# Kernel tuning notes

Measured on AMD Instinct MI355X. Metric: run time of the kernel, lower is better.

The kernel has to match this reference:

```python
import jax, jax.numpy as jnp
import numpy as np

B, NCOL, NCOND = 1024, 64, 64
NRODT, D, NEST, NFOREST, NHID, NCLASS = 1024, 4, 128, 100, 128, 10
EPS = 1e-5


def setup_inputs() -> dict:
    key = jax.random.key(0)
    ks = jax.random.split(key, 16)
    rng = np.random.default_rng(0)
    s = 0.1
    inp = {
        'x': jax.random.normal(ks[0], (B, NCOL), jnp.float32),
        # phi_1 numerical grouped conv: groups=NCOL, in_per_g=1, out_per_g=NCOND
        'w1': jax.random.normal(ks[1], (NCOL, 1, NCOND), jnp.float32) * s,
        'b1': jax.random.normal(ks[2], (NCOL * NCOND,), jnp.float32) * s,
        # rODTConstruction fixed permutation of the 4096 conditions
        'perm': jnp.asarray(rng.permutation(NCOND * NCOL), jnp.int32),
        'gn1_g': jnp.ones((NCOND * NCOL,), jnp.float32),
        'gn1_b': jnp.zeros((NCOND * NCOL,), jnp.float32),
        # phi_2 grouped convs: groups=NRODT, block D->D then D->1
        'w2a': jax.random.normal(ks[3], (NRODT, D, D), jnp.float32) * s,
        'b2a': jax.random.normal(ks[4], (NRODT * D,), jnp.float32) * s,
        'gn2_g': jnp.ones((NCOND * NCOL,), jnp.float32),
        'gn2_b': jnp.zeros((NCOND * NCOL,), jnp.float32),
        'w2b': jax.random.normal(ks[5], (NRODT, D, 1), jnp.float32) * s,
        'b2b': jax.random.normal(ks[6], (NRODT,), jnp.float32) * s,
        'E': jax.random.normal(ks[7], (NRODT, NHID), jnp.float32) * s,
        # eval-mode sample_without_replacement buffer: per-forest subset of rODTs
        'swr': jnp.asarray(np.argsort(rng.random((NFOREST, NRODT)), axis=-1)[:, :NEST], jnp.int32),
        'ln1_g': jnp.ones((NHID,), jnp.float32),
        'ln1_b': jnp.zeros((NHID,), jnp.float32),
        'lin1_w': jax.random.normal(ks[8], (NHID, NHID), jnp.float32) * s,
        'lin1_b': jax.random.normal(ks[9], (NHID,), jnp.float32) * s,
        'ln2_g': jnp.ones((NHID,), jnp.float32),
        'ln2_b': jnp.zeros((NHID,), jnp.float32),
        'lin2_w': jax.random.normal(ks[10], (NHID, NCLASS), jnp.float32) * s,
        'lin2_b': jax.random.normal(ks[11], (NCLASS,), jnp.float32) * s,
    }
    return inp


def _group_norm(v, g, gamma, beta):
    # v: (B, C), normalize within each of g channel groups (L=1 in the torch module)
    b, c = v.shape
    vg = v.reshape(b, g, c // g)
    mu = vg.mean(-1, keepdims=True)
    var = vg.var(-1, keepdims=True)
    vn = ((vg - mu) / jnp.sqrt(var + EPS)).reshape(b, c)
    return vn * gamma + beta


def _layer_norm(v, gamma, beta):
    mu = v.mean(-1, keepdims=True)
    var = v.var(-1, keepdims=True)
    return (v - mu) / jnp.sqrt(var + EPS) * gamma + beta


def reference(x, w1, b1, perm, gn1_g, gn1_b, w2a, b2a, gn2_g, gn2_b, w2b, b2b,
              E, swr, ln1_g, ln1_b, lin1_w, lin1_b, ln2_g, ln2_b, lin2_w, lin2_b):
    b = x.shape[0]
    # ConditionGeneration (numerical only): block-diag GEMV with in_per_group=1
    M = jax.nn.sigmoid(x[:, :, None] * w1[None, :, 0, :] + b1.reshape(NCOL, NCOND))  # (B, NCOL, NCOND)
    M = M.transpose(0, 2, 1)  # (B, NCOND, NCOL)
    # rODTConstruction: flatten + fixed permutation
    O = M.reshape(b, NCOND * NCOL)[:, perm]  # (B, 4096)
    # phi_2: GroupNorm -> grouped conv (D->D) -> ReLU -> GroupNorm -> grouped conv (D->1)
    h = _group_norm(O, NRODT, gn1_g, gn1_b).reshape(b, NRODT, D)
    h = jnp.einsum('bgi,gio->bgo', h, w2a) + b2a.reshape(NRODT, D)
    h = jax.nn.relu(h).reshape(b, NRODT * D)
    h = _group_norm(h, NRODT, gn2_g, gn2_b).reshape(b, NRODT, D)
    w = jnp.einsum('bgi,gio->bgo', h, w2b)[..., 0] + b2b  # (B, NRODT), n_head=1
    # forest construction: gather rODT subsets, softmax over estimators, weighted embed sum
    ws = jax.nn.softmax(w[:, swr], axis=-1)  # (B, NFOREST, NEST)
    Es = E[swr]  # (NFOREST, NEST, NHID)
    F = jnp.einsum('bfe,feh->bfh', ws, Es)  # (B, NFOREST, NHID)
    # phi_3 bagging MLP (eval mode: dropout = identity)
    z = _layer_norm(F, ln1_g, ln1_b)
    z = jax.nn.relu(z @ lin1_w + lin1_b)
    z = _layer_norm(z, ln2_g, ln2_b)
    y_hats = z @ lin2_w + lin2_b  # (B, NFOREST, NCLASS)
    return y_hats.mean(1)  # (B, NCLASS)
```

## Files before the change

### kernel.cpp

```cpp
#include <hip/hip_runtime.h>


#define B_      1024
#define NCOL_   64
#define NCOND_  64
#define NRODT_  1024
#define NEST_   128
#define NFOREST_ 100
#define NHID_   128
#define NCLASS_ 10
#define EPS_    1e-5f

typedef __bf16 bf16_t;
typedef bf16_t bf16x8 __attribute__((ext_vector_type(8)));
typedef float  f32x4  __attribute__((ext_vector_type(4)));

#define MFMA16(a,b,c) __builtin_amdgcn_mfma_f32_16x16x32_bf16(a,b,c,0,0,0)

#define EG_FRAGS   (NFOREST_*4*8*64)
#define W1_FRAGS   (4*8*64)
#define L2_FRAGS   (4*64)

#define ZLD 136

__global__ __launch_bounds__(256) void k_prep(
    const float* __restrict__ E,     const int*   __restrict__ swr,
    const float* __restrict__ lin1w, const float* __restrict__ lin2w,
    const float* __restrict__ x,
    bf16_t* __restrict__ Eh,  bf16_t* __restrict__ El,
    bf16_t* __restrict__ Wh,  bf16_t* __restrict__ Wl,
    bf16_t* __restrict__ L2h, bf16_t* __restrict__ L2l,
    float*  __restrict__ x_t, float* __restrict__ accz)
{
    int blk = blockIdx.x, tid = threadIdx.x;
    if (blk < 800) {
        int t = blk * 256 + tid;
        int lane = t & 63, nn = (t >> 6) & 7, kk = (t >> 9) & 3, f = t >> 11;
        int q = lane >> 4, n = nn * 16 + (lane & 15);
        bf16x8 hi, lo;
#pragma unroll
        for (int j = 0; j < 8; ++j) {
            int e = kk * 32 + q * 8 + j;
            int r = swr[f * NEST_ + e];
            float v = E[r * NHID_ + n];
            bf16_t h = (bf16_t)v;
            hi[j] = h; lo[j] = (bf16_t)(v - (float)h);
        }
        *(bf16x8*)(Eh + (size_t)t * 8) = hi;
        *(bf16x8*)(El + (size_t)t * 8) = lo;
    } else if (blk < 808) {
        int t = (blk - 800) * 256 + tid;
        int lane = t & 63, nn = (t >> 6) & 7, kk = t >> 9;
        int q = lane >> 4, n = nn * 16 + (lane & 15);
        bf16x8 hi, lo;
#pragma unroll
        for (int j = 0; j < 8; ++j) {
            int k = kk * 32 + q * 8 + j;
            float v = lin1w[k * NHID_ + n];
            bf16_t h = (bf16_t)v;
            hi[j] = h; lo[j] = (bf16_t)(v - (float)h);
        }
        *(bf16x8*)(Wh + t * 8) = hi;
        *(bf16x8*)(Wl + t * 8) = lo;
    } else if (blk == 808) {
        int t = tid;
        int lane = t & 63, kk = t >> 6;
        int q = lane >> 4, n = lane & 15;
        bf16x8 hi, lo;
#pragma unroll
        for (int j = 0; j < 8; ++j) {
            int k = kk * 32 + q * 8 + j;
            float v = (n < NCLASS_) ? lin2w[k * NCLASS_ + n] : 0.f;
            bf16_t h = (bf16_t)v;
            hi[j] = h; lo[j] = (bf16_t)(v - (float)h);
        }
        *(bf16x8*)(L2h + t * 8) = hi;
        *(bf16x8*)(L2l + t * 8) = lo;
    } else if (blk < 1065) {
        int t = (blk - 809) * 256 + tid;
        x_t[t] = x[(t & 1023) * NCOL_ + (t >> 10)];
    } else {
        int t = (blk - 1065) * 256 + tid;
        if (t < B_ * NCLASS_) accz[t] = 0.f;
    }
}

__global__ __launch_bounds__(256) void k_rodt(
    const float* __restrict__ x_t,  const float* __restrict__ w1,
    const float* __restrict__ b1,   const int*  __restrict__ perm,
    const float* __restrict__ gn1g, const float* __restrict__ gn1b,
    const float* __restrict__ w2a,  const float* __restrict__ b2a,
    const float* __restrict__ gn2g, const float* __restrict__ gn2b,
    const float* __restrict__ w2b,  const float* __restrict__ b2b,
    float* __restrict__ w_t)
{
    int g  = blockIdx.x;
    int bq = threadIdx.x * 4;

    int4 p4 = ((const int4*)perm)[g];
    int col[4]  = { p4.x & 63, p4.y & 63, p4.z & 63, p4.w & 63 };
    int cond[4] = { p4.x >> 6, p4.y >> 6, p4.z >> 6, p4.w >> 6 };
    float w1v[4], b1v[4];
#pragma unroll
    for (int j = 0; j < 4; ++j) {
        w1v[j] = w1[col[j] * NCOND_ + cond[j]];
        b1v[j] = b1[col[j] * NCOND_ + cond[j]];
    }
    float4 g1  = ((const float4*)gn1g)[g];
    float4 o1  = ((const float4*)gn1b)[g];
    float4 ba  = ((const float4*)b2a)[g];
    float4 g2  = ((const float4*)gn2g)[g];
    float4 o2  = ((const float4*)gn2b)[g];
    float4 wb4 = ((const float4*)w2b)[g];
    float  bb  = b2b[g];
    float4 wa[4];
    const float4* w2a4 = (const float4*)w2a;
#pragma unroll
    for (int i = 0; i < 4; ++i) wa[i] = w2a4[g * 4 + i];

    float xv[4][4];
#pragma unroll
    for (int j = 0; j < 4; ++j) {
        float4 t = *(const float4*)&x_t[col[j] * B_ + bq];
        xv[j][0] = t.x; xv[j][1] = t.y; xv[j][2] = t.z; xv[j][3] = t.w;
    }

    float outv[4];
#pragma unroll
    for (int bi = 0; bi < 4; ++bi) {
        float v[4];
#pragma unroll
        for (int j = 0; j < 4; ++j) {
            float t = xv[j][bi] * w1v[j] + b1v[j];
            v[j] = 1.0f / (1.0f + __expf(-t));
        }
        float mu = (v[0] + v[1] + v[2] + v[3]) * 0.25f;
        float var = 0.f;
#pragma unroll
        for (int j = 0; j < 4; ++j) { float d = v[j] - mu; var += d * d; }
        var *= 0.25f;
        float rs = rsqrtf(var + EPS_);
        float h[4];
        h[0] = (v[0] - mu) * rs * g1.x + o1.x;
        h[1] = (v[1] - mu) * rs * g1.y + o1.y;
        h[2] = (v[2] - mu) * rs * g1.z + o1.z;
        h[3] = (v[3] - mu) * rs * g1.w + o1.w;

        float4 a = ba;
#pragma unroll
        for (int i = 0; i < 4; ++i) {
            a.x += h[i] * wa[i].x; a.y += h[i] * wa[i].y;
            a.z += h[i] * wa[i].z; a.w += h[i] * wa[i].w;
        }
        float t2[4];
        t2[0] = fmaxf(a.x, 0.f); t2[1] = fmaxf(a.y, 0.f);
        t2[2] = fmaxf(a.z, 0.f); t2[3] = fmaxf(a.w, 0.f);

        float mu2 = (t2[0] + t2[1] + t2[2] + t2[3]) * 0.25f;
        float var2 = 0.f;
#pragma unroll
        for (int j = 0; j < 4; ++j) { float d = t2[j] - mu2; var2 += d * d; }
        var2 *= 0.25f;
        float rs2 = rsqrtf(var2 + EPS_);

        float wvv = bb;
        wvv += ((t2[0] - mu2) * rs2 * g2.x + o2.x) * wb4.x;
        wvv += ((t2[1] - mu2) * rs2 * g2.y + o2.y) * wb4.y;
        wvv += ((t2[2] - mu2) * rs2 * g2.z + o2.z) * wb4.z;
        wvv += ((t2[3] - mu2) * rs2 * g2.w + o2.w) * wb4.w;
        outv[bi] = wvv;
    }
    *(float4*)&w_t[(size_t)g * B_ + bq] = make_float4(outv[0], outv[1], outv[2], outv[3]);
}

__global__ __launch_bounds__(256) void k_forest(
    const float*  __restrict__ w_t, const int* __restrict__ swr,
    const bf16_t* __restrict__ Eh,  const bf16_t* __restrict__ El,
    const bf16_t* __restrict__ Wh,  const bf16_t* __restrict__ Wl,
    const bf16_t* __restrict__ L2h, const bf16_t* __restrict__ L2l,
    const float* __restrict__ ln1g, const float* __restrict__ ln1b,
    const float* __restrict__ lin1b,
    const float* __restrict__ ln2g, const float* __restrict__ ln2b,
    float* __restrict__ acc)
{
    __shared__ __align__(16) float  zC[64 * 132];
    __shared__ __align__(16) bf16_t zb[64 * ZLD];

    int tid  = threadIdx.x;
    int wid  = tid >> 6;
    int lane = tid & 63;
    int q    = lane >> 4;
    int mc   = lane & 15;

    int n    = blockIdx.x;
    int swiz = (n & 7) * 200 + (n >> 3);
    int f    = swiz >> 4;
    int bt   = swiz & 15;
    int b0   = bt * 64 + wid * 16;

    const int* swrf = swr + f * NEST_;
    int nn0 = wid * 2;

    float ex[4][8];
    float mx = -1e30f;
#pragma unroll
    for (int kk = 0; kk < 4; ++kk) {
        int4 r0 = *(const int4*)(swrf + kk * 32 + q * 8);
        int4 r1 = *(const int4*)(swrf + kk * 32 + q * 8 + 4);
        int rr[8] = { r0.x, r0.y, r0.z, r0.w, r1.x, r1.y, r1.z, r1.w };
#pragma unroll
        for (int j = 0; j < 8; ++j) {
            float v = w_t[rr[j] * B_ + b0 + mc];
            ex[kk][j] = v;
            mx = fmaxf(mx, v);
        }
    }
    mx = fmaxf(mx, __shfl_xor(mx, 16));
    mx = fmaxf(mx, __shfl_xor(mx, 32));
    float s = 0.f;
#pragma unroll
    for (int kk = 0; kk < 4; ++kk)
#pragma unroll
        for (int j = 0; j < 8; ++j) { ex[kk][j] = __expf(ex[kk][j] - mx); s += ex[kk][j]; }
    s += __shfl_xor(s, 16);
    s += __shfl_xor(s, 32);
    float inv = 1.f / s;

#pragma unroll
    for (int kk = 0; kk < 4; ++kk) {
        bf16x8 v;
#pragma unroll
        for (int j = 0; j < 8; ++j) v[j] = (bf16_t)(ex[kk][j] * inv);
        *(bf16x8*)&zb[(wid * 16 + mc) * ZLD + kk * 32 + q * 8] = v;
    }

    __syncthreads();

    const bf16x8* EHf = (const bf16x8*)Eh;
    const bf16x8* ELf = (const bf16x8*)El;
    f32x4 accF[4][2];
#pragma unroll
    for (int mt = 0; mt < 4; ++mt) {
        accF[mt][0] = (f32x4){0.f, 0.f, 0.f, 0.f};
        accF[mt][1] = (f32x4){0.f, 0.f, 0.f, 0.f};
    }
#pragma unroll
    for (int kk = 0; kk < 4; ++kk) {
        size_t bi = (size_t)(f * 4 + kk) * 8;
        bf16x8 bh0 = EHf[(bi + nn0) * 64 + lane];
        bf16x8 bh1 = EHf[(bi + nn0 + 1) * 64 + lane];
        bf16x8 bl0 = ELf[(bi + nn0) * 64 + lane];
        bf16x8 bl1 = ELf[(bi + nn0 + 1) * 64 + lane];
        bf16x8 av[4];
#pragma unroll
        for (int mt = 0; mt < 4; ++mt)
            av[mt] = *(const bf16x8*)&zb[(mt * 16 + mc) * ZLD + kk * 32 + q * 8];
#pragma unroll
        for (int mt = 0; mt < 4; ++mt) {
            accF[mt][0] = MFMA16(av[mt], bh0, accF[mt][0]);
            accF[mt][1] = MFMA16(av[mt], bh1, accF[mt][1]);
            accF[mt][0] = MFMA16(av[mt], bl0, accF[mt][0]);
            accF[mt][1] = MFMA16(av[mt], bl1, accF[mt][1]);
        }
    }
#pragma unroll
    for (int mt = 0; mt < 4; ++mt)
#pragma unroll
        for (int nj = 0; nj < 2; ++nj)
#pragma unroll
            for (int reg = 0; reg < 4; ++reg)
                zC[(mt * 16 + q * 4 + reg) * 132 + (nn0 + nj) * 16 + mc] = accF[mt][nj][reg];

    __syncthreads();

    {
        float vv[8][4];
#pragma unroll
        for (int nn = 0; nn < 8; ++nn)
#pragma unroll
            for (int reg = 0; reg < 4; ++reg)
                vv[nn][reg] = zC[(wid * 16 + q * 4 + reg) * 132 + nn * 16 + mc];
        float mu[4], rs[4];
#pragma unroll
        for (int reg = 0; reg < 4; ++reg) {
            float ps = 0.f, pq = 0.f;
#pragma unroll
            for (int nn = 0; nn < 8; ++nn) { float v = vv[nn][reg]; ps += v; pq += v * v; }
#pragma unroll
            for (int o = 1; o <= 8; o <<= 1) { ps += __shfl_xor(ps, o); pq += __shfl_xor(pq, o); }
            float m_ = ps * (1.f / NHID_);
            mu[reg] = m_;
            rs[reg] = rsqrtf(pq * (1.f / NHID_) - m_ * m_ + EPS_);
        }
#pragma unroll
        for (int nn = 0; nn < 8; ++nn) {
            int c = nn * 16 + mc;
            float gv = ln1g[c], bv = ln1b[c];
#pragma unroll
            for (int reg = 0; reg < 4; ++reg)
                zb[(wid * 16 + q * 4 + reg) * ZLD + c] =
                    (bf16_t)((vv[nn][reg] - mu[reg]) * rs[reg] * gv + bv);
        }
    }

    __syncthreads();

    const bf16x8* WHf = (const bf16x8*)Wh;
    const bf16x8* WLf = (const bf16x8*)Wl;
    f32x4 accA[4][2];
#pragma unroll
    for (int mt = 0; mt < 4; ++mt) {
        accA[mt][0] = (f32x4){0.f, 0.f, 0.f, 0.f};
        accA[mt][1] = (f32x4){0.f, 0.f, 0.f, 0.f};
    }
#pragma unroll
    for (int kk = 0; kk < 4; ++kk) {
        bf16x8 bh0 = WHf[(kk * 8 + nn0) * 64 + lane];
        bf16x8 bh1 = WHf[(kk * 8 + nn0 + 1) * 64 + lane];
        bf16x8 bl0 = WLf[(kk * 8 + nn0) * 64 + lane];
        bf16x8 bl1 = WLf[(kk * 8 + nn0 + 1) * 64 + lane];
        bf16x8 av[4];
#pragma unroll
        for (int mt = 0; mt < 4; ++mt)
            av[mt] = *(const bf16x8*)&zb[(mt * 16 + mc) * ZLD + kk * 32 + q * 8];
#pragma unroll
        for (int mt = 0; mt < 4; ++mt) {
            accA[mt][0] = MFMA16(av[mt], bh0, accA[mt][0]);
            accA[mt][1] = MFMA16(av[mt], bh1, accA[mt][1]);
            accA[mt][0] = MFMA16(av[mt], bl0, accA[mt][0]);
            accA[mt][1] = MFMA16(av[mt], bl1, accA[mt][1]);
        }
    }

    __syncthreads();
#pragma unroll
    for (int mt = 0; mt < 4; ++mt)
#pragma unroll
        for (int nj = 0; nj < 2; ++nj)
#pragma unroll
            for (int reg = 0; reg < 4; ++reg)
                zC[(mt * 16 + q * 4 + reg) * 132 + (nn0 + nj) * 16 + mc] = accA[mt][nj][reg];

    __syncthreads();

    {
        float vv[8][4];
#pragma unroll
        for (int nn = 0; nn < 8; ++nn) {
            float bv = lin1b[nn * 16 + mc];
#pragma unroll
            for (int reg = 0; reg < 4; ++reg)
                vv[nn][reg] = fmaxf(
                    zC[(wid * 16 + q * 4 + reg) * 132 + nn * 16 + mc] + bv, 0.f);
        }
        float mu2[4], rs2[4];
#pragma unroll
        for (int reg = 0; reg < 4; ++reg) {
            float ps = 0.f, pq = 0.f;
#pragma unroll
            for (int nn = 0; nn < 8; ++nn) { float v = vv[nn][reg]; ps += v; pq += v * v; }
#pragma unroll
            for (int o = 1; o <= 8; o <<= 1) { ps += __shfl_xor(ps, o); pq += __shfl_xor(pq, o); }
            float m_ = ps * (1.f / NHID_);
            mu2[reg] = m_;
            rs2[reg] = rsqrtf(pq * (1.f / NHID_) - m_ * m_ + EPS_);
        }
#pragma unroll
        for (int nn = 0; nn < 8; ++nn) {
            int c = nn * 16 + mc;
            float gv = ln2g[c], bv = ln2b[c];
#pragma unroll
            for (int reg = 0; reg < 4; ++reg)
                zb[(wid * 16 + q * 4 + reg) * ZLD + c] =
                    (bf16_t)((vv[nn][reg] - mu2[reg]) * rs2[reg] * gv + bv);
        }
    }

    f32x4 accO = {0.f, 0.f, 0.f, 0.f};
    const bf16x8* LHf = (const bf16x8*)L2h;
    const bf16x8* LLf = (const bf16x8*)L2l;
#pragma unroll
    for (int kk = 0; kk < 4; ++kk) {
        bf16x8 a3 = *(const bf16x8*)&zb[(wid * 16 + mc) * ZLD + kk * 32 + q * 8];
        accO = MFMA16(a3, LHf[kk * 64 + lane], accO);
        accO = MFMA16(a3, LLf[kk * 64 + lane], accO);
    }
    if (mc < NCLASS_) {
#pragma unroll
        for (int reg = 0; reg < 4; ++reg)
            atomicAdd(&acc[(b0 + q * 4 + reg) * NCLASS_ + mc], accO[reg]);
    }
}

__global__ __launch_bounds__(256) void k_final(
    const float* __restrict__ acc, const float* __restrict__ lin2b,
    float* __restrict__ out)
{
    int i = blockIdx.x * 256 + threadIdx.x;
    if (i < B_ * NCLASS_) {
        int c = i % NCLASS_;
        out[i] = acc[i] * (1.f / NFOREST_) + lin2b[c];
    }
}

extern "C" void kernel_launch(void* const* d_in, const int* in_sizes, int n_in,
                              void* d_out, int out_size, void* d_ws, size_t ws_size,
                              hipStream_t stream)
{
    const float* x     = (const float*)d_in[0];
    const float* w1    = (const float*)d_in[1];
    const float* b1    = (const float*)d_in[2];
    const int*   perm  = (const int*)  d_in[3];
    const float* gn1g  = (const float*)d_in[4];
    const float* gn1b  = (const float*)d_in[5];
    const float* w2a   = (const float*)d_in[6];
    const float* b2a   = (const float*)d_in[7];
    const float* gn2g  = (const float*)d_in[8];
    const float* gn2b  = (const float*)d_in[9];
    const float* w2b   = (const float*)d_in[10];
    const float* b2b   = (const float*)d_in[11];
    const float* E     = (const float*)d_in[12];
    const int*   swr   = (const int*)  d_in[13];
    const float* ln1g  = (const float*)d_in[14];
    const float* ln1b  = (const float*)d_in[15];
    const float* lin1w = (const float*)d_in[16];
    const float* lin1b = (const float*)d_in[17];
    const float* ln2g  = (const float*)d_in[18];
    const float* ln2b  = (const float*)d_in[19];
    const float* lin2w = (const float*)d_in[20];
    const float* lin2b = (const float*)d_in[21];

    char* base = (char*)d_ws;
    float*  w_t  = (float*)base;
    float*  accp = (float*)(base + 4u * 1024 * 1024);
    float*  x_t  = (float*)(base + 4u * 1024 * 1024 + 64 * 1024);
    bf16_t* Eh   = (bf16_t*)(base + 4u * 1024 * 1024 + 64 * 1024 + 256 * 1024);
    bf16_t* El   = Eh  + (size_t)EG_FRAGS * 8;
    bf16_t* Wh   = El  + (size_t)EG_FRAGS * 8;
    bf16_t* Wl   = Wh  + (size_t)W1_FRAGS * 8;
    bf16_t* L2h  = Wl  + (size_t)W1_FRAGS * 8;
    bf16_t* L2l  = L2h + (size_t)L2_FRAGS * 8;

    k_prep<<<1105, 256, 0, stream>>>(E, swr, lin1w, lin2w, x,
                                     Eh, El, Wh, Wl, L2h, L2l, x_t, accp);

    k_rodt<<<NRODT_, 256, 0, stream>>>(
        x_t, w1, b1, perm, gn1g, gn1b, w2a, b2a, gn2g, gn2b, w2b, b2b, w_t);

    k_forest<<<NFOREST_ * 16, 256, 0, stream>>>(
        w_t, swr, Eh, El, Wh, Wl, L2h, L2l,
        ln1g, ln1b, lin1b, ln2g, ln2b, accp);

    k_final<<<(B_ * NCLASS_ + 255) / 256, 256, 0, stream>>>(
        accp, lin2b, (float*)d_out);
}
```

Before: 141.6 us.

## Fuse layernorms into MFMA registers, prefetch weights, drop final kernel

Removes the zC fp32 staging tile. Each layernorm is now computed directly from MFMA accumulators, with per-row partial sums exchanged through a small shared pstat array, which cuts LDS traffic and one barrier per norm. E and lin1 weight fragments are double-buffered in registers so global loads overlap the MFMAs, and launch_bounds(256,4) sets an occupancy target. The k_final kernel is removed: the prep kernel writes lin2b into the output and the forest kernel atomically adds pre-scaled partials, saving a launch at the cost of a different float summation order.

```diff
diff --git a/kernel.cpp b/kernel.cpp
--- a/kernel.cpp
+++ b/kernel.cpp
@@ -26,11 +26,11 @@
 __global__ __launch_bounds__(256) void k_prep(
     const float* __restrict__ E,     const int*   __restrict__ swr,
     const float* __restrict__ lin1w, const float* __restrict__ lin2w,
-    const float* __restrict__ x,
+    const float* __restrict__ x,     const float* __restrict__ lin2b,
     bf16_t* __restrict__ Eh,  bf16_t* __restrict__ El,
     bf16_t* __restrict__ Wh,  bf16_t* __restrict__ Wl,
     bf16_t* __restrict__ L2h, bf16_t* __restrict__ L2l,
-    float*  __restrict__ x_t, float* __restrict__ accz)
+    float*  __restrict__ x_t, float* __restrict__ out)
 {
     int blk = blockIdx.x, tid = threadIdx.x;
     if (blk < 800) {
@@ -81,7 +81,7 @@
         x_t[t] = x[(t & 1023) * NCOL_ + (t >> 10)];
     } else {
         int t = (blk - 1065) * 256 + tid;
-        if (t < B_ * NCLASS_) accz[t] = 0.f;
+        if (t < B_ * NCLASS_) out[t] = lin2b[t % NCLASS_];
     }
 }
 
@@ -173,7 +173,7 @@
     *(float4*)&w_t[(size_t)g * B_ + bq] = make_float4(outv[0], outv[1], outv[2], outv[3]);
 }
 
-__global__ __launch_bounds__(256) void k_forest(
+__global__ __launch_bounds__(256, 4) void k_forest(
     const float*  __restrict__ w_t, const int* __restrict__ swr,
     const bf16_t* __restrict__ Eh,  const bf16_t* __restrict__ El,
     const bf16_t* __restrict__ Wh,  const bf16_t* __restrict__ Wl,
@@ -181,10 +181,10 @@
     const float* __restrict__ ln1g, const float* __restrict__ ln1b,
     const float* __restrict__ lin1b,
     const float* __restrict__ ln2g, const float* __restrict__ ln2b,
-    float* __restrict__ acc)
+    float* __restrict__ out)
 {
-    __shared__ __align__(16) float  zC[64 * 132];
     __shared__ __align__(16) bf16_t zb[64 * ZLD];
+    __shared__ __align__(8)  float2 pstat[4][64];
 
     int tid  = threadIdx.x;
     int wid  = tid >> 6;
@@ -201,6 +201,13 @@
     const int* swrf = swr + f * NEST_;
     int nn0 = wid * 2;
 
+    const bf16x8* EHf = (const bf16x8*)Eh;
+    const bf16x8* ELf = (const bf16x8*)El;
+    const bf16x8* WHf = (const bf16x8*)Wh;
+    const bf16x8* WLf = (const bf16x8*)Wl;
+    const bf16x8* LHf = (const bf16x8*)L2h;
+    const bf16x8* LLf = (const bf16x8*)L2l;
+
     float ex[4][8];
     float mx = -1e30f;
 #pragma unroll
@@ -215,6 +222,16 @@
             mx = fmaxf(mx, v);
         }
     }
+
+    bf16x8 peA0, peA1, peA2, peA3;
+    {
+        size_t bi = (size_t)(f * 4 + 0) * 8;
+        peA0 = EHf[(bi + nn0) * 64 + lane];
+        peA1 = EHf[(bi + nn0 + 1) * 64 + lane];
+        peA2 = ELf[(bi + nn0) * 64 + lane];
+        peA3 = ELf[(bi + nn0 + 1) * 64 + lane];
+    }
+
     mx = fmaxf(mx, __shfl_xor(mx, 16));
     mx = fmaxf(mx, __shfl_xor(mx, 32));
     float s = 0.f;
@@ -236,171 +253,190 @@
 
     __syncthreads();
 
-    const bf16x8* EHf = (const bf16x8*)Eh;
-    const bf16x8* ELf = (const bf16x8*)El;
     f32x4 accF[4][2];
 #pragma unroll
     for (int mt = 0; mt < 4; ++mt) {
         accF[mt][0] = (f32x4){0.f, 0.f, 0.f, 0.f};
         accF[mt][1] = (f32x4){0.f, 0.f, 0.f, 0.f};
     }
-#pragma unroll
-    for (int kk = 0; kk < 4; ++kk) {
-        size_t bi = (size_t)(f * 4 + kk) * 8;
-        bf16x8 bh0 = EHf[(bi + nn0) * 64 + lane];
-        bf16x8 bh1 = EHf[(bi + nn0 + 1) * 64 + lane];
-        bf16x8 bl0 = ELf[(bi + nn0) * 64 + lane];
-        bf16x8 bl1 = ELf[(bi + nn0 + 1) * 64 + lane];
-        bf16x8 av[4];
+    bf16x8 peB0, peB1, peB2, peB3;
+
+#define LOAD_E(d0, d1, d2, d3, KK) { \
+        size_t bi_ = (size_t)(f * 4 + (KK)) * 8; \
+        d0 = EHf[(bi_ + nn0) * 64 + lane]; \
+        d1 = EHf[(bi_ + nn0 + 1) * 64 + lane]; \
+        d2 = ELf[(bi_ + nn0) * 64 + lane]; \
+        d3 = ELf[(bi_ + nn0 + 1) * 64 + lane]; }
+
+#define FSTEP(P0_, P1_, P2_, P3_, KK) { \
+        bf16x8 av[4]; \
+        _Pragma("unroll") \
+        for (int mt = 0; mt < 4; ++mt) \
+            av[mt] = *(const bf16x8*)&zb[(mt * 16 + mc) * ZLD + (KK) * 32 + q * 8]; \
+        _Pragma("unroll") \
+        for (int mt = 0; mt < 4; ++mt) { \
+            accF[mt][0] = MFMA16(av[mt], P0_, accF[mt][0]); \
+            accF[mt][1] = MFMA16(av[mt], P1_, accF[mt][1]); \
+            accF[mt][0] = MFMA16(av[mt], P2_, accF[mt][0]); \
+            accF[mt][1] = MFMA16(av[mt], P3_, accF[mt][1]); } }
+
+    LOAD_E(peB0, peB1, peB2, peB3, 1);
+    FSTEP(peA0, peA1, peA2, peA3, 0);
+    LOAD_E(peA0, peA1, peA2, peA3, 2);
+    FSTEP(peB0, peB1, peB2, peB3, 1);
+    LOAD_E(peB0, peB1, peB2, peB3, 3);
+    FSTEP(peA0, peA1, peA2, peA3, 2);
+    FSTEP(peB0, peB1, peB2, peB3, 3);
+
+#pragma unroll
+    for (int mt = 0; mt < 4; ++mt)
+#pragma unroll
+        for (int reg = 0; reg < 4; ++reg) {
+            float a0 = accF[mt][0][reg], a1 = accF[mt][1][reg];
+            float sp = a0 + a1;
+            float qp = a0 * a0 + a1 * a1;
+#pragma unroll
+            for (int o = 1; o <= 8; o <<= 1) { sp += __shfl_xor(sp, o); qp += __shfl_xor(qp, o); }
+            if (mc == 0) pstat[wid][mt * 16 + q * 4 + reg] = make_float2(sp, qp);
+        }
+
+    bf16x8 pwA0, pwA1, pwA2, pwA3;
+    pwA0 = WHf[(0 * 8 + nn0) * 64 + lane];
+    pwA1 = WHf[(0 * 8 + nn0 + 1) * 64 + lane];
+    pwA2 = WLf[(0 * 8 + nn0) * 64 + lane];
+    pwA3 = WLf[(0 * 8 + nn0 + 1) * 64 + lane];
+
+    __syncthreads();
+
+    {
+        float gv0 = ln1g[nn0 * 16 + mc],      bv0 = ln1b[nn0 * 16 + mc];
+        float gv1 = ln1g[nn0 * 16 + 16 + mc], bv1 = ln1b[nn0 * 16 + 16 + mc];
 #pragma unroll
         for (int mt = 0; mt < 4; ++mt)
-            av[mt] = *(const bf16x8*)&zb[(mt * 16 + mc) * ZLD + kk * 32 + q * 8];
-#pragma unroll
-        for (int mt = 0; mt < 4; ++mt) {
-            accF[mt][0] = MFMA16(av[mt], bh0, accF[mt][0]);
-            accF[mt][1] = MFMA16(av[mt], bh1, accF[mt][1]);
-            accF[mt][0] = MFMA16(av[mt], bl0, accF[mt][0]);
-            accF[mt][1] = MFMA16(av[mt], bl1, accF[mt][1]);
-        }
-    }
-#pragma unroll
-    for (int mt = 0; mt < 4; ++mt)
-#pragma unroll
-        for (int nj = 0; nj < 2; ++nj)
-#pragma unroll
-            for (int reg = 0; reg < 4; ++reg)
-                zC[(mt * 16 + q * 4 + reg) * 132 + (nn0 + nj) * 16 + mc] = accF[mt][nj][reg];
+#pragma unroll
+            for (int reg = 0; reg < 4; ++reg) {
+                int r = mt * 16 + q * 4 + reg;
+                float2 p0 = pstat[0][r], p1 = pstat[1][r];
+                float2 p2 = pstat[2][r], p3 = pstat[3][r];
+                float sv = (p0.x + p1.x) + (p2.x + p3.x);
+                float qv = (p0.y + p1.y) + (p2.y + p3.y);
+                float m_ = sv * (1.f / NHID_);
+                float rv = rsqrtf(qv * (1.f / NHID_) - m_ * m_ + EPS_);
+                zb[r * ZLD + nn0 * 16 + mc] =
+                    (bf16_t)((accF[mt][0][reg] - m_) * rv * gv0 + bv0);
+                zb[r * ZLD + nn0 * 16 + 16 + mc] =
+                    (bf16_t)((accF[mt][1][reg] - m_) * rv * gv1 + bv1);
+            }
+    }
 
     __syncthreads();
 
-    {
-        float vv[8][4];
-#pragma unroll
-        for (int nn = 0; nn < 8; ++nn)
-#pragma unroll
-            for (int reg = 0; reg < 4; ++reg)
-                vv[nn][reg] = zC[(wid * 16 + q * 4 + reg) * 132 + nn * 16 + mc];
-        float mu[4], rs[4];
-#pragma unroll
-        for (int reg = 0; reg < 4; ++reg) {
-            float ps = 0.f, pq = 0.f;
-#pragma unroll
-            for (int nn = 0; nn < 8; ++nn) { float v = vv[nn][reg]; ps += v; pq += v * v; }
-#pragma unroll
-            for (int o = 1; o <= 8; o <<= 1) { ps += __shfl_xor(ps, o); pq += __shfl_xor(pq, o); }
-            float m_ = ps * (1.f / NHID_);
-            mu[reg] = m_;
-            rs[reg] = rsqrtf(pq * (1.f / NHID_) - m_ * m_ + EPS_);
-        }
-#pragma unroll
-        for (int nn = 0; nn < 8; ++nn) {
-            int c = nn * 16 + mc;
-            float gv = ln1g[c], bv = ln1b[c];
-#pragma unroll
-            for (int reg = 0; reg < 4; ++reg)
-                zb[(wid * 16 + q * 4 + reg) * ZLD + c] =
-                    (bf16_t)((vv[nn][reg] - mu[reg]) * rs[reg] * gv + bv);
-        }
-    }
-
-    __syncthreads();
-
-    const bf16x8* WHf = (const bf16x8*)Wh;
-    const bf16x8* WLf = (const bf16x8*)Wl;
     f32x4 accA[4][2];
 #pragma unroll
     for (int mt = 0; mt < 4; ++mt) {
         accA[mt][0] = (f32x4){0.f, 0.f, 0.f, 0.f};
         accA[mt][1] = (f32x4){0.f, 0.f, 0.f, 0.f};
     }
+    bf16x8 pwB0, pwB1, pwB2, pwB3;
+
+#define LOAD_W(d0, d1, d2, d3, KK) { \
+        d0 = WHf[((KK) * 8 + nn0) * 64 + lane]; \
+        d1 = WHf[((KK) * 8 + nn0 + 1) * 64 + lane]; \
+        d2 = WLf[((KK) * 8 + nn0) * 64 + lane]; \
+        d3 = WLf[((KK) * 8 + nn0 + 1) * 64 + lane]; }
+
+#define ASTEP(P0_, P1_, P2_, P3_, KK) { \
+        bf16x8 av[4]; \
+        _Pragma("unroll") \
+        for (int mt = 0; mt < 4; ++mt) \
+            av[mt] = *(const bf16x8*)&zb[(mt * 16 + mc) * ZLD + (KK) * 32 + q * 8]; \
+        _Pragma("unroll") \
+        for (int mt = 0; mt < 4; ++mt) { \
+            accA[mt][0] = MFMA16(av[mt], P0_, accA[mt][0]); \
+            accA[mt][1] = MFMA16(av[mt], P1_, accA[mt][1]); \
+            accA[mt][0] = MFMA16(av[mt], P2_, accA[mt][0]); \
+            accA[mt][1] = MFMA16(av[mt], P3_, accA[mt][1]); } }
+
+    LOAD_W(pwB0, pwB1, pwB2, pwB3, 1);
+    ASTEP(pwA0, pwA1, pwA2, pwA3, 0);
+    LOAD_W(pwA0, pwA1, pwA2, pwA3, 2);
+    ASTEP(pwB0, pwB1, pwB2, pwB3, 1);
+    LOAD_W(pwB0, pwB1, pwB2, pwB3, 3);
+    ASTEP(pwA0, pwA1, pwA2, pwA3, 2);
+    ASTEP(pwB0, pwB1, pwB2, pwB3, 3);
+
+    {
+        float bb0 = lin1b[nn0 * 16 + mc];
+        float bb1 = lin1b[nn0 * 16 + 16 + mc];
+#pragma unroll
+        for (int mt = 0; mt < 4; ++mt)
+#pragma unroll
+            for (int reg = 0; reg < 4; ++reg) {
+                accA[mt][0][reg] = fmaxf(accA[mt][0][reg] + bb0, 0.f);
+                accA[mt][1][reg] = fmaxf(accA[mt][1][reg] + bb1, 0.f);
+            }
+    }
+#pragma unroll
+    for (int mt = 0; mt < 4; ++mt)
+#pragma unroll
+        for (int reg = 0; reg < 4; ++reg) {
+            float a0 = accA[mt][0][reg], a1 = accA[mt][1][reg];
+            float sp = a0 + a1;
+            float qp = a0 * a0 + a1 * a1;
+#pragma unroll
+            for (int o = 1; o <= 8; o <<= 1) { sp += __shfl_xor(sp, o); qp += __shfl_xor(qp, o); }
+            if (mc == 0) pstat[wid][mt * 16 + q * 4 + reg] = make_float2(sp, qp);
+        }
+
+    bf16x8 pl2[4][2];
 #pragma unroll
     for (int kk = 0; kk < 4; ++kk) {
-        bf16x8 bh0 = WHf[(kk * 8 + nn0) * 64 + lane];
-        bf16x8 bh1 = WHf[(kk * 8 + nn0 + 1) * 64 + lane];
-        bf16x8 bl0 = WLf[(kk * 8 + nn0) * 64 + lane];
-        bf16x8 bl1 = WLf[(kk * 8 + nn0 + 1) * 64 + lane];
-        bf16x8 av[4];
+        pl2[kk][0] = LHf[kk * 64 + lane];
+        pl2[kk][1] = LLf[kk * 64 + lane];
+    }
+
+    __syncthreads();
+
+    {
+        float gv0 = ln2g[nn0 * 16 + mc],      bv0 = ln2b[nn0 * 16 + mc];
+        float gv1 = ln2g[nn0 * 16 + 16 + mc], bv1 = ln2b[nn0 * 16 + 16 + mc];
 #pragma unroll
         for (int mt = 0; mt < 4; ++mt)
-            av[mt] = *(const bf16x8*)&zb[(mt * 16 + mc) * ZLD + kk * 32 + q * 8];
-#pragma unroll
-        for (int mt = 0; mt < 4; ++mt) {
-            accA[mt][0] = MFMA16(av[mt], bh0, accA[mt][0]);
-            accA[mt][1] = MFMA16(av[mt], bh1, accA[mt][1]);
-            accA[mt][0] = MFMA16(av[mt], bl0, accA[mt][0]);
-            accA[mt][1] = MFMA16(av[mt], bl1, accA[mt][1]);
-        }
+#pragma unroll
+            for (int reg = 0; reg < 4; ++reg) {
+                int r = mt * 16 + q * 4 + reg;
+                float2 p0 = pstat[0][r], p1 = pstat[1][r];
+                float2 p2 = pstat[2][r], p3 = pstat[3][r];
+                float sv = (p0.x + p1.x) + (p2.x + p3.x);
+                float qv = (p0.y + p1.y) + (p2.y + p3.y);
+                float m_ = sv * (1.f / NHID_);
+                float rv = rsqrtf(qv * (1.f / NHID_) - m_ * m_ + EPS_);
+                zb[r * ZLD + nn0 * 16 + mc] =
+                    (bf16_t)((accA[mt][0][reg] - m_) * rv * gv0 + bv0);
+                zb[r * ZLD + nn0 * 16 + 16 + mc] =
+                    (bf16_t)((accA[mt][1][reg] - m_) * rv * gv1 + bv1);
+            }
     }
 
     __syncthreads();
-#pragma unroll
-    for (int mt = 0; mt < 4; ++mt)
-#pragma unroll
-        for (int nj = 0; nj < 2; ++nj)
-#pragma unroll
-            for (int reg = 0; reg < 4; ++reg)
-                zC[(mt * 16 + q * 4 + reg) * 132 + (nn0 + nj) * 16 + mc] = accA[mt][nj][reg];
-
-    __syncthreads();
-
-    {
-        float vv[8][4];
-#pragma unroll
-        for (int nn = 0; nn < 8; ++nn) {
-            float bv = lin1b[nn * 16 + mc];
-#pragma unroll
-            for (int reg = 0; reg < 4; ++reg)
-                vv[nn][reg] = fmaxf(
-                    zC[(wid * 16 + q * 4 + reg) * 132 + nn * 16 + mc] + bv, 0.f);
-        }
-        float mu2[4], rs2[4];
-#pragma unroll
-        for (int reg = 0; reg < 4; ++reg) {
-            float ps = 0.f, pq = 0.f;
-#pragma unroll
-            for (int nn = 0; nn < 8; ++nn) { float v = vv[nn][reg]; ps += v; pq += v * v; }
-#pragma unroll
-            for (int o = 1; o <= 8; o <<= 1) { ps += __shfl_xor(ps, o); pq += __shfl_xor(pq, o); }
-            float m_ = ps * (1.f / NHID_);
-            mu2[reg] = m_;
-            rs2[reg] = rsqrtf(pq * (1.f / NHID_) - m_ * m_ + EPS_);
-        }
-#pragma unroll
-        for (int nn = 0; nn < 8; ++nn) {
-            int c = nn * 16 + mc;
-            float gv = ln2g[c], bv = ln2b[c];
-#pragma unroll
-            for (int reg = 0; reg < 4; ++reg)
-                zb[(wid * 16 + q * 4 + reg) * ZLD + c] =
-                    (bf16_t)((vv[nn][reg] - mu2[reg]) * rs2[reg] * gv + bv);
-        }
-    }
 
     f32x4 accO = {0.f, 0.f, 0.f, 0.f};
-    const bf16x8* LHf = (const bf16x8*)L2h;
-    const bf16x8* LLf = (const bf16x8*)L2l;
 #pragma unroll
     for (int kk = 0; kk < 4; ++kk) {
         bf16x8 a3 = *(const bf16x8*)&zb[(wid * 16 + mc) * ZLD + kk * 32 + q * 8];
-        accO = MFMA16(a3, LHf[kk * 64 + lane], accO);
-        accO = MFMA16(a3, LLf[kk * 64 + lane], accO);
+        accO = MFMA16(a3, pl2[kk][0], accO);
+        accO = MFMA16(a3, pl2[kk][1], accO);
     }
     if (mc < NCLASS_) {
 #pragma unroll
         for (int reg = 0; reg < 4; ++reg)
-            atomicAdd(&acc[(b0 + q * 4 + reg) * NCLASS_ + mc], accO[reg]);
-    }
-}
-
-__global__ __launch_bounds__(256) void k_final(
-    const float* __restrict__ acc, const float* __restrict__ lin2b,
-    float* __restrict__ out)
-{
-    int i = blockIdx.x * 256 + threadIdx.x;
-    if (i < B_ * NCLASS_) {
-        int c = i % NCLASS_;
-        out[i] = acc[i] * (1.f / NFOREST_) + lin2b[c];
-    }
+            atomicAdd(&out[(b0 + q * 4 + reg) * NCLASS_ + mc],
+                      accO[reg] * (1.f / NFOREST_));
+    }
+#undef LOAD_E
+#undef FSTEP
+#undef LOAD_W
+#undef ASTEP
 }
 
 extern "C" void kernel_launch(void* const* d_in, const int* in_sizes, int n_in,
@@ -432,7 +468,6 @@
 
     char* base = (char*)d_ws;
     float*  w_t  = (float*)base;
-    float*  accp = (float*)(base + 4u * 1024 * 1024);
     float*  x_t  = (float*)(base + 4u * 1024 * 1024 + 64 * 1024);
     bf16_t* Eh   = (bf16_t*)(base + 4u * 1024 * 1024 + 64 * 1024 + 256 * 1024);
     bf16_t* El   = Eh  + (size_t)EG_FRAGS * 8;
@@ -441,16 +476,14 @@
     bf16_t* L2h  = Wl  + (size_t)W1_FRAGS * 8;
     bf16_t* L2l  = L2h + (size_t)L2_FRAGS * 8;
 
-    k_prep<<<1105, 256, 0, stream>>>(E, swr, lin1w, lin2w, x,
-                                     Eh, El, Wh, Wl, L2h, L2l, x_t, accp);
+    k_prep<<<1105, 256, 0, stream>>>(E, swr, lin1w, lin2w, x, lin2b,
+                                     Eh, El, Wh, Wl, L2h, L2l, x_t,
+                                     (float*)d_out);
 
     k_rodt<<<NRODT_, 256, 0, stream>>>(
         x_t, w1, b1, perm, gn1g, gn1b, w2a, b2a, gn2g, gn2b, w2b, b2b, w_t);
 
     k_forest<<<NFOREST_ * 16, 256, 0, stream>>>(
         w_t, swr, Eh, El, Wh, Wl, L2h, L2l,
-        ln1g, ln1b, lin1b, ln2g, ln2b, accp);
-
-    k_final<<<(B_ * NCLASS_ + 255) / 256, 256, 0, stream>>>(
-        accp, lin2b, (float*)d_out);
+        ln1g, ln1b, lin1b, ln2g, ln2b, (float*)d_out);
 }
```

Result: slower. 155.2 us (+9.6%).
